# Kernel optimization log

Hardware: AMD Instinct MI355X
Metric: run time of the kernel (lower is better)

## Reference

```python
import jax, jax.numpy as jnp
import numpy as np

N = 50000
E = 800000
DIM = 256
HEADS = 4
HDIM = DIM // HEADS  # 64
NEG_SLOPE = 0.2
LN_EPS = 1e-5


def _layernorm(x, g, b):
    mu = jnp.mean(x, axis=-1, keepdims=True)
    var = jnp.var(x, axis=-1, keepdims=True)
    return (x - mu) * jax.lax.rsqrt(var + LN_EPS) * g + b


def setup_inputs() -> dict:
    key = jax.random.key(0)
    ks = jax.random.split(key, 10)
    x = jax.random.normal(ks[0], (N, DIM), dtype=jnp.float32)
    edge_index = jax.random.randint(ks[1], (2, E), 0, N, dtype=jnp.int64)
    s = 0.05
    W = jax.random.normal(ks[2], (DIM, DIM), dtype=jnp.float32) * s       # GAT linear (heads*out = dim)
    a_src = jax.random.normal(ks[3], (HEADS, HDIM), dtype=jnp.float32) * s
    a_dst = jax.random.normal(ks[4], (HEADS, HDIM), dtype=jnp.float32) * s
    gat_b = jnp.zeros((DIM,), dtype=jnp.float32)
    ln_g = jnp.ones((DIM,), dtype=jnp.float32)
    ln_b = jnp.zeros((DIM,), dtype=jnp.float32)
    W1 = jax.random.normal(ks[5], (DIM, 4 * DIM), dtype=jnp.float32) * s
    b1 = jnp.zeros((4 * DIM,), dtype=jnp.float32)
    W2 = jax.random.normal(ks[6], (4 * DIM, DIM), dtype=jnp.float32) * s
    b2 = jnp.zeros((DIM,), dtype=jnp.float32)
    return {"x": x, "edge_index": edge_index, "W": W, "a_src": a_src,
            "a_dst": a_dst, "gat_b": gat_b, "ln_g": ln_g, "ln_b": ln_b,
            "W1": W1, "b1": b1, "W2": W2, "b2": b2}


def _gat(x, edge_index, W, a_src, a_dst, gat_b):
    # project and split heads: [N, H, C]
    h = (x @ W).reshape(N, HEADS, HDIM)
    alpha_src = jnp.einsum('nhc,hc->nh', h, a_src)  # [N, H]
    alpha_dst = jnp.einsum('nhc,hc->nh', h, a_dst)  # [N, H]
    src = edge_index[0]
    dst = edge_index[1]
    e = jax.nn.leaky_relu(alpha_src[src] + alpha_dst[dst], NEG_SLOPE)  # [E, H]
    # segment softmax over edges sharing a destination node
    m = jax.ops.segment_max(e, dst, num_segments=N)                   # [N, H]
    ex = jnp.exp(e - m[dst])
    denom = jax.ops.segment_sum(ex, dst, num_segments=N)              # [N, H]
    alpha = ex / (denom[dst] + 1e-16)                                 # [E, H]
    msg = h[src] * alpha[:, :, None]                                  # [E, H, C]
    out = jax.ops.segment_sum(msg.reshape(E, DIM), dst, num_segments=N)
    return out + gat_b


def reference(x, edge_index, W, a_src, a_dst, gat_b, ln_g, ln_b, W1, b1, W2, b2):
    residual = x
    g = _gat(x, edge_index, W, a_src, a_dst, gat_b)
    x = _layernorm(x + g, ln_g, ln_b)
    ffn = jax.nn.gelu(x @ W1 + b1, approximate=False) @ W2 + b2
    x = _layernorm(x + ffn, ln_g, ln_b)  # same norm params reused, as in source
    return x + residual
```

## Files before the change

### kernel.cpp

```cpp
#include <hip/hip_runtime.h>
#include <hip/hip_bf16.h>
#include <math.h>

typedef __bf16 bf16;
typedef bf16 bf16x8 __attribute__((ext_vector_type(8)));
typedef float floatx4 __attribute__((ext_vector_type(4)));

#define NN 50000
#define EE 800000
#define DIMC 256
#define FFC 1024

typedef __attribute__((address_space(3))) unsigned int lds_u32;
typedef __attribute__((address_space(1))) unsigned int gbl_u32;

static __device__ __forceinline__ void glds16(const bf16* g, bf16* l) {
    __builtin_amdgcn_global_load_lds((const gbl_u32*)g, (lds_u32*)l, 16, 0, 0);
}

static __device__ __forceinline__ unsigned short f2b(float f) {
    bf16 b = (bf16)f;
    return __builtin_bit_cast(unsigned short, b);
}
static __device__ __forceinline__ float b2f_lo(unsigned u) { return __uint_as_float(u << 16); }
static __device__ __forceinline__ float b2f_hi(unsigned u) { return __uint_as_float(u & 0xffff0000u); }

static __device__ __forceinline__ float gelu_f(float v) {
    float z = -1.5957691216f * v - 0.0713548163f * v * v * v;
    return v / (1.f + __expf(z));
}

__global__ __launch_bounds__(256)
void k_cast_bf16(const float* __restrict__ in, bf16* __restrict__ out, long n4) {
    long i = (long)blockIdx.x * 256 + threadIdx.x;
    if (i >= n4) return;
    float4 v = ((const float4*)in)[i];
    uint2 p;
    p.x = (unsigned)f2b(v.x) | ((unsigned)f2b(v.y) << 16);
    p.y = (unsigned)f2b(v.z) | ((unsigned)f2b(v.w) << 16);
    ((uint2*)out)[i] = p;
}

__global__ __launch_bounds__(256)
void k_tcast(const float* __restrict__ in, bf16* __restrict__ out, int K, int Nc) {
    __shared__ float t[32][33];
    int n0 = blockIdx.x * 32, k0 = blockIdx.y * 32;
    int tx = threadIdx.x & 31, ty = threadIdx.x >> 5;
#pragma unroll
    for (int i = 0; i < 4; ++i)
        t[ty + i * 8][tx] = in[(long)(k0 + ty + i * 8) * Nc + n0 + tx];
    __syncthreads();
#pragma unroll
    for (int i = 0; i < 4; ++i)
        out[(long)(n0 + ty + i * 8) * K + k0 + tx] = (bf16)t[tx][ty + i * 8];
}

template <int EPI>
__global__ __launch_bounds__(256)
void k_gemmA(const bf16* __restrict__ A, const bf16* __restrict__ BT,
             bf16* __restrict__ C, const float* __restrict__ bias,
             const float* __restrict__ avs, const float* __restrict__ avd,
             float* __restrict__ asrcO, float* __restrict__ adstO,
             int M, int K, int Nc) {
    __shared__ __attribute__((aligned(16))) bf16 smem[17408];
    bf16* As = smem;
    bf16* Bs = smem + 8192;
    const int tid = threadIdx.x;
    const int w = tid >> 6, lane = tid & 63;
    const int gm = blockIdx.x * 128, gn = blockIdx.y * 128;
    const int wm = (w >> 1) * 64, wn = (w & 1) * 64;
    const int lr = lane & 15, lkc = lane >> 4;

    long aoff[4], boff[4];
#pragma unroll
    for (int j = 0; j < 4; ++j) {
        int s = w * 4 + j;
        int r = s * 8 + (lane >> 3);
        int kc = ((lane & 7) ^ (r & 7)) * 8;
        aoff[j] = (long)min(gm + r, M - 1) * K + kc;
        boff[j] = (long)(gn + r) * K + kc;
    }

    floatx4 acc[4][4];
#pragma unroll
    for (int a = 0; a < 4; ++a)
#pragma unroll
        for (int b = 0; b < 4; ++b) acc[a][b] = floatx4{0.f, 0.f, 0.f, 0.f};

    for (int k0 = 0; k0 < K; k0 += 64) {
        if (k0) __syncthreads();
#pragma unroll
        for (int j = 0; j < 4; ++j) {
            int s = w * 4 + j;
            glds16(A + aoff[j] + k0, As + s * 512);
            glds16(BT + boff[j] + k0, Bs + s * 512);
        }
        __syncthreads();
#pragma unroll
        for (int kk = 0; kk < 2; ++kk) {
            bf16x8 af[4], bv[4];
#pragma unroll
            for (int mi = 0; mi < 4; ++mi) {
                int r = wm + mi * 16 + lr;
                int ch = (kk * 4 + lkc) ^ (r & 7);
                af[mi] = *(const bf16x8*)(As + r * 64 + ch * 8);
            }
#pragma unroll
            for (int ni = 0; ni < 4; ++ni) {
                int r = wn + ni * 16 + lr;
                int ch = (kk * 4 + lkc) ^ (r & 7);
                bv[ni] = *(const bf16x8*)(Bs + r * 64 + ch * 8);
            }
#pragma unroll
            for (int mi = 0; mi < 4; ++mi)
#pragma unroll
                for (int ni = 0; ni < 4; ++ni)
                    acc[mi][ni] = __builtin_amdgcn_mfma_f32_16x16x32_bf16(af[mi], bv[ni], acc[mi][ni], 0, 0, 0);
        }
    }

    __syncthreads();
    bf16* cs = smem;
#pragma unroll
    for (int ni = 0; ni < 4; ++ni) {
        const int cl = wn + ni * 16 + lr;
        const float bvs = (EPI == 1) ? bias[gn + cl] : 0.f;
#pragma unroll
        for (int mi = 0; mi < 4; ++mi)
#pragma unroll
            for (int i = 0; i < 4; ++i) {
                int rl = wm + mi * 16 + lkc * 4 + i;
                float v = acc[mi][ni][i] + bvs;
                if (EPI == 1) v = gelu_f(v);
                cs[rl * 136 + cl] = (bf16)v;
            }
    }
    __syncthreads();

    const int c8 = (lane & 15) * 8;
    float as8[8], ad8[8];
    int hd = 0;
    if (EPI == 0) {
        hd = (gn >> 6) + ((lane & 15) >> 3);
        const int cb = hd * 64 + (c8 & 63);
#pragma unroll
        for (int i = 0; i < 8; ++i) { as8[i] = avs[cb + i]; ad8[i] = avd[cb + i]; }
    }

#pragma unroll
    for (int t = 0; t < 8; ++t) {
        int rl = w * 32 + t * 4 + (lane >> 4);
        int grow = gm + rl;
        uint4 val = *(const uint4*)(cs + rl * 136 + c8);
        if (grow < M) *(uint4*)(C + (long)grow * Nc + gn + c8) = val;
        if (EPI == 0) {
            float h0 = b2f_lo(val.x), h1 = b2f_hi(val.x), h2 = b2f_lo(val.y), h3 = b2f_hi(val.y);
            float h4 = b2f_lo(val.z), h5 = b2f_hi(val.z), h6 = b2f_lo(val.w), h7 = b2f_hi(val.w);
            float ds = h0 * as8[0] + h1 * as8[1] + h2 * as8[2] + h3 * as8[3]
                     + h4 * as8[4] + h5 * as8[5] + h6 * as8[6] + h7 * as8[7];
            float dd = h0 * ad8[0] + h1 * ad8[1] + h2 * ad8[2] + h3 * ad8[3]
                     + h4 * ad8[4] + h5 * ad8[5] + h6 * ad8[6] + h7 * ad8[7];
#pragma unroll
            for (int off = 1; off < 8; off <<= 1) { ds += __shfl_xor(ds, off); dd += __shfl_xor(dd, off); }
            if ((lane & 7) == 0 && grow < M) {
                asrcO[grow * 4 + hd] = ds;
                adstO[grow * 4 + hd] = dd;
            }
        }
    }
}

__global__ __launch_bounds__(512)
void k_ffn(const bf16* __restrict__ x1b, const bf16* __restrict__ W1T,
           const bf16* __restrict__ W2T, const float* __restrict__ b1,
           const float* __restrict__ b2, const float* __restrict__ x,
           const float* __restrict__ lng, const float* __restrict__ lnb,
           float* __restrict__ out, int M) {
    __shared__ __attribute__((aligned(16))) bf16 smem[20480];
    float* actf = (float*)smem;
    bf16* w1s = smem + 4096;
    bf16* w2s = smem + 12288;
    const int tid = threadIdx.x;
    const int w = tid >> 6, lane = tid & 63;
    const int lr = lane & 15, lkc = lane >> 4;
    const int mg = w >> 1, nh = w & 1;
    const int gm = blockIdx.x * 64;

    bf16x8 xf[8];
    {
        long rb = (long)min(gm + mg * 16 + lr, M - 1) * DIMC;
#pragma unroll
        for (int kf = 0; kf < 8; ++kf)
            xf[kf] = *(const bf16x8*)(x1b + rb + kf * 32 + lkc * 8);
    }

    floatx4 accB[8];
#pragma unroll
    for (int i = 0; i < 8; ++i) accB[i] = floatx4{0.f, 0.f, 0.f, 0.f};

    const int rbA = nh * 16 + lr;
    const int rAct = mg * 16 + lr;
    const int kAct = nh * 16 + lr;

    for (int c = 0; c < 32; ++c) {
        if (c) __syncthreads();
#pragma unroll
        for (int j = 0; j < 2; ++j) {
            int sg = w * 2 + j;
            int r = sg * 2 + (lane >> 5);
            int col = ((lane & 31) ^ (r & 7)) * 8;
            glds16(W1T + (long)(c * 32 + r) * DIMC + col, w1s + sg * 512);
        }
#pragma unroll
        for (int j = 0; j < 2; ++j) {
            int sg = w * 2 + j;
            int r = sg * 16 + (lane >> 2);
            int col = c * 32 + (((lane & 3) ^ ((r >> 1) & 3)) * 8);
            glds16(W2T + (long)r * FFC + col, w2s + sg * 512);
        }
        __syncthreads();

        floatx4 a0 = floatx4{0.f, 0.f, 0.f, 0.f}, a1 = a0;
#pragma unroll
        for (int kf = 0; kf < 8; kf += 2) {
            int g0 = (kf * 4 + lkc) ^ (rbA & 7);
            int g1 = ((kf + 1) * 4 + lkc) ^ (rbA & 7);
            bf16x8 bva = *(const bf16x8*)(w1s + rbA * 256 + g0 * 8);
            bf16x8 bvb = *(const bf16x8*)(w1s + rbA * 256 + g1 * 8);
            a0 = __builtin_amdgcn_mfma_f32_16x16x32_bf16(xf[kf], bva, a0, 0, 0, 0);
            a1 = __builtin_amdgcn_mfma_f32_16x16x32_bf16(xf[kf + 1], bvb, a1, 0, 0, 0);
        }
        float b1v = b1[c * 32 + kAct];
#pragma unroll
        for (int i = 0; i < 4; ++i) {
            int r = mg * 16 + lkc * 4 + i;
            float v = gelu_f(a0[i] + a1[i] + b1v);
            actf[r * 32 + (((kAct >> 2) ^ (r & 7)) << 2) + (kAct & 3)] = v;
        }
        __syncthreads();

        {
            int g0 = (lkc * 2) ^ (rAct & 7);
            int g1 = (lkc * 2 + 1) ^ (rAct & 7);
            float4 lo = *(const float4*)(actf + rAct * 32 + g0 * 4);
            float4 hi = *(const float4*)(actf + rAct * 32 + g1 * 4);
            bf16x8 af;
            af[0] = (bf16)lo.x; af[1] = (bf16)lo.y; af[2] = (bf16)lo.z; af[3] = (bf16)lo.w;
            af[4] = (bf16)hi.x; af[5] = (bf16)hi.y; af[6] = (bf16)hi.z; af[7] = (bf16)hi.w;
#pragma unroll
            for (int ni = 0; ni < 8; ++ni) {
                int rb = nh * 128 + ni * 16 + lr;
                int gb = lkc ^ ((rb >> 1) & 3);
                bf16x8 bv = *(const bf16x8*)(w2s + rb * 32 + gb * 8);
                accB[ni] = __builtin_amdgcn_mfma_f32_16x16x32_bf16(af, bv, accB[ni], 0, 0, 0);
            }
        }
    }

    __syncthreads();
    bf16* cs = smem;
#pragma unroll
    for (int ni = 0; ni < 8; ++ni) {
        int col = nh * 128 + ni * 16 + lr;
        float b2v = b2[col];
#pragma unroll
        for (int i = 0; i < 4; ++i) {
            int rl = mg * 16 + lkc * 4 + i;
            cs[rl * 264 + col] = (bf16)(accB[ni][i] + b2v);
        }
    }
    __syncthreads();
    float4 g4 = *(const float4*)(lng + lane * 4);
    float4 lb4 = *(const float4*)(lnb + lane * 4);
#pragma unroll 1
    for (int t = 0; t < 8; ++t) {
        int r = w * 8 + t;
        int grow = gm + r;
        long base = (long)min(grow, M - 1) * DIMC + lane * 4;
        uint2 cu = *(const uint2*)(cs + r * 264 + lane * 4);
        uint2 xu = *(const uint2*)(x1b + base);
        float v0 = b2f_lo(cu.x) + b2f_lo(xu.x);
        float v1 = b2f_hi(cu.x) + b2f_hi(xu.x);
        float v2 = b2f_lo(cu.y) + b2f_lo(xu.y);
        float v3 = b2f_hi(cu.y) + b2f_hi(xu.y);
        float s1 = v0 + v1 + v2 + v3;
        float s2 = v0 * v0 + v1 * v1 + v2 * v2 + v3 * v3;
#pragma unroll
        for (int off = 1; off < 64; off <<= 1) { s1 += __shfl_xor(s1, off); s2 += __shfl_xor(s2, off); }
        float mu = s1 * (1.f / DIMC);
        float rs = rsqrtf(s2 * (1.f / DIMC) - mu * mu + 1e-5f);
        float4 xr = *(const float4*)(x + base);
        float4 o;
        o.x = (v0 - mu) * rs * g4.x + lb4.x + xr.x;
        o.y = (v1 - mu) * rs * g4.y + lb4.y + xr.y;
        o.z = (v2 - mu) * rs * g4.z + lb4.z + xr.z;
        o.w = (v3 - mu) * rs * g4.w + lb4.w + xr.w;
        if (grow < M) *(float4*)(out + (long)grow * DIMC + lane * 4) = o;
    }
}

__global__ __launch_bounds__(256)
void k_count(const int* __restrict__ dst, unsigned* __restrict__ deg) {
    int e = blockIdx.x * 256 + threadIdx.x;
    if (e < EE) atomicAdd(&deg[dst[e]], 1u);
}

__global__ __launch_bounds__(1024)
void k_scan(const unsigned* __restrict__ deg, unsigned* __restrict__ rowoff,
            unsigned* __restrict__ cursor) {
    __shared__ unsigned wsum[16], wscan[16];
    __shared__ unsigned carry;
    int tid = threadIdx.x, lane = tid & 63, wid = tid >> 6;
    if (tid == 0) carry = 0;
    __syncthreads();
    for (int base = 0; base < NN; base += 1024) {
        int i = base + tid;
        unsigned v = (i < NN) ? deg[i] : 0u;
        unsigned s = v;
        for (int off = 1; off < 64; off <<= 1) {
            unsigned t = __shfl_up(s, off);
            if (lane >= off) s += t;
        }
        if (lane == 63) wsum[wid] = s;
        __syncthreads();
        if (wid == 0) {
            unsigned t = (lane < 16) ? wsum[lane] : 0u;
            unsigned ts = t;
            for (int off = 1; off < 16; off <<= 1) {
                unsigned u2 = __shfl_up(ts, off);
                if (lane >= off) ts += u2;
            }
            if (lane < 16) wscan[lane] = ts;
        }
        __syncthreads();
        unsigned basew = (wid > 0) ? wscan[wid - 1] : 0u;
        unsigned excl = carry + basew + (s - v);
        if (i < NN) { rowoff[i] = excl; cursor[i] = excl; }
        __syncthreads();
        if (tid == 0) carry += wscan[15];
        __syncthreads();
    }
    if (tid == 0) rowoff[NN] = carry;
}

__global__ __launch_bounds__(256)
void k_fill(const int* __restrict__ src, const int* __restrict__ dst,
            unsigned* __restrict__ cursor, unsigned* __restrict__ elist) {
    int e = blockIdx.x * 256 + threadIdx.x;
    if (e < EE) {
        unsigned p = atomicAdd(&cursor[dst[e]], 1u);
        elist[p] = (unsigned)src[e];
    }
}

__global__ __launch_bounds__(256)
void k_agg_ln1(const unsigned* __restrict__ rowoff, const unsigned* __restrict__ elist,
               const float* __restrict__ asrc, const float* __restrict__ adst,
               const bf16* __restrict__ hb, const float* __restrict__ x,
               const float* __restrict__ gatb, const float* __restrict__ lng,
               const float* __restrict__ lnb, bf16* __restrict__ x1b) {
    int node = (blockIdx.x * 256 + threadIdx.x) >> 6;
    int lane = threadIdx.x & 63;
    if (node >= NN) return;
    int beg = (int)rowoff[node], end = (int)rowoff[node + 1];
    int head = lane >> 4;
    float ad = adst[node * 4 + head];
    const int c = lane * 4;
    const bf16* hc = hb + c;
    const int bl = lane & 48;

    float dsum = 0.f;
    float a0 = 0.f, a1 = 0.f, a2 = 0.f, a3 = 0.f;

    for (int c0 = beg; c0 < end; c0 += 16) {
        int take = end - c0; if (take > 16) take = 16;
        int jj = c0 + (lane & 15);
        float ex = 0.f; int s = 0;
        if (jj < end) {
            s = (int)elist[jj];
            float e = asrc[s * 4 + head] + ad;
            e = (e > 0.f) ? e : 0.2f * e;
            ex = __expf(e);
        }
        dsum += ex;
        if (take == 16) {
#pragma unroll
            for (int j = 0; j < 16; ++j) {
                float al = __shfl(ex, bl + j);
                int sj = __shfl(s, bl + j);
                uint2 u = *(const uint2*)(hc + (long)sj * DIMC);
                a0 += al * b2f_lo(u.x);
                a1 += al * b2f_hi(u.x);
                a2 += al * b2f_lo(u.y);
                a3 += al * b2f_hi(u.y);
            }
        } else {
            for (int j = 0; j < take; ++j) {
                float al = __shfl(ex, bl + j);
                int sj = __shfl(s, bl + j);
                uint2 u = *(const uint2*)(hc + (long)sj * DIMC);
                a0 += al * b2f_lo(u.x);
                a1 += al * b2f_hi(u.x);
                a2 += al * b2f_lo(u.y);
                a3 += al * b2f_hi(u.y);
            }
        }
    }
    dsum += __shfl_xor(dsum, 1);
    dsum += __shfl_xor(dsum, 2);
    dsum += __shfl_xor(dsum, 4);
    dsum += __shfl_xor(dsum, 8);
    float invd = 1.f / (dsum + 1e-16f);
    a0 *= invd; a1 *= invd; a2 *= invd; a3 *= invd;

    long base = (long)node * DIMC + c;
    float4 xr = *(const float4*)(x + base);
    float4 gb = *(const float4*)(gatb + c);
    float v0 = xr.x + a0 + gb.x;
    float v1 = xr.y + a1 + gb.y;
    float v2 = xr.z + a2 + gb.z;
    float v3 = xr.w + a3 + gb.w;
    float s1 = v0 + v1 + v2 + v3;
    float s2 = v0 * v0 + v1 * v1 + v2 * v2 + v3 * v3;
    for (int off = 1; off < 64; off <<= 1) { s1 += __shfl_xor(s1, off); s2 += __shfl_xor(s2, off); }
    float mu = s1 * (1.f / DIMC);
    float rs = rsqrtf(s2 * (1.f / DIMC) - mu * mu + 1e-5f);
    float4 g4 = *(const float4*)(lng + c);
    float4 b4 = *(const float4*)(lnb + c);
    float y0 = (v0 - mu) * rs * g4.x + b4.x;
    float y1 = (v1 - mu) * rs * g4.y + b4.y;
    float y2 = (v2 - mu) * rs * g4.z + b4.z;
    float y3 = (v3 - mu) * rs * g4.w + b4.w;
    uint2 p;
    p.x = (unsigned)f2b(y0) | ((unsigned)f2b(y1) << 16);
    p.y = (unsigned)f2b(y2) | ((unsigned)f2b(y3) << 16);
    *(uint2*)(x1b + base) = p;
}

extern "C" void kernel_launch(void* const* d_in, const int* in_sizes, int n_in,
                              void* d_out, int out_size, void* d_ws, size_t ws_size,
                              hipStream_t stream) {
    const float* x    = (const float*)d_in[0];
    const int*   ei   = (const int*)d_in[1];
    const float* W    = (const float*)d_in[2];
    const float* a_s  = (const float*)d_in[3];
    const float* a_d  = (const float*)d_in[4];
    const float* gatb = (const float*)d_in[5];
    const float* lng  = (const float*)d_in[6];
    const float* lnb  = (const float*)d_in[7];
    const float* W1   = (const float*)d_in[8];
    const float* b1   = (const float*)d_in[9];
    const float* W2   = (const float*)d_in[10];
    const float* b2   = (const float*)d_in[11];
    float* out = (float*)d_out;
    char* ws = (char*)d_ws;

    bf16*     xb     = (bf16*)(ws + 0L);
    bf16*     hb     = (bf16*)(ws + 25600000L);
    bf16*     x1b    = (bf16*)(ws + 51200000L);
    float*    asrc   = (float*)(ws + 179200000L);
    float*    adst   = (float*)(ws + 180000000L);
    unsigned* deg    = (unsigned*)(ws + 180800000L);
    unsigned* cursor = (unsigned*)(ws + 181000192L);
    unsigned* rowoff = (unsigned*)(ws + 181200384L);
    unsigned* elist  = (unsigned*)(ws + 181400832L);
    bf16*     WT     = (bf16*)(ws + 184600832L);
    bf16*     W1T    = (bf16*)(ws + 184731904L);
    bf16*     W2T    = (bf16*)(ws + 185256192L);

    const int* esrc = ei;
    const int* edst = ei + EE;

    hipMemsetAsync(deg, 0, NN * sizeof(unsigned), stream);
    k_cast_bf16<<<12500, 256, 0, stream>>>(x, xb, (long)NN * DIMC / 4);
    {
        dim3 gw(DIMC / 32, DIMC / 32);
        k_tcast<<<gw, 256, 0, stream>>>(W, WT, DIMC, DIMC);
        dim3 gw1(FFC / 32, DIMC / 32);
        k_tcast<<<gw1, 256, 0, stream>>>(W1, W1T, DIMC, FFC);
        dim3 gw2(DIMC / 32, FFC / 32);
        k_tcast<<<gw2, 256, 0, stream>>>(W2, W2T, FFC, DIMC);
    }

    dim3 g1(391, 2);
    k_gemmA<0><<<g1, 256, 0, stream>>>(xb, WT, hb, nullptr, a_s, a_d, asrc, adst, NN, DIMC, DIMC);

    k_count<<<3125, 256, 0, stream>>>(edst, deg);
    k_scan<<<1, 1024, 0, stream>>>(deg, rowoff, cursor);
    k_fill<<<3125, 256, 0, stream>>>(esrc, edst, cursor, elist);

    k_agg_ln1<<<12500, 256, 0, stream>>>(rowoff, elist, asrc, adst, hb, x, gatb, lng, lnb, x1b);

    k_ffn<<<782, 512, 0, stream>>>(x1b, W1T, W2T, b1, b2, x, lng, lnb, out, NN);
}
```

Before: 500.9 us.

## Fuse degree count into cast, merge weight transposes, parallelize CSR scan

Folds the per-edge degree atomics into the bf16 cast kernel and merges the three weight-transpose launches into one grid with block-index dispatch. The single-block serial scan over 50000 nodes becomes a three-phase multi-block scan: per-block scan, block-sum scan, then an offset add. This removes several launches and the long single-workgroup scan, at the cost of two extra small kernels and extra rowoff/cursor read-modify-write traffic.

Result: faster. 442.2 us (-11.7%).

```diff
diff --git a/kernel.cpp b/kernel.cpp
--- a/kernel.cpp
+++ b/kernel.cpp
@@ -31,8 +31,10 @@
 }
 
 __global__ __launch_bounds__(256)
-void k_cast_bf16(const float* __restrict__ in, bf16* __restrict__ out, long n4) {
+void k_cast_count(const float* __restrict__ in, bf16* __restrict__ out, long n4,
+                  const int* __restrict__ dst, unsigned* __restrict__ deg) {
     long i = (long)blockIdx.x * 256 + threadIdx.x;
+    if (i < EE) atomicAdd(&deg[dst[(int)i]], 1u);
     if (i >= n4) return;
     float4 v = ((const float4*)in)[i];
     uint2 p;
@@ -42,9 +44,16 @@
 }
 
 __global__ __launch_bounds__(256)
-void k_tcast(const float* __restrict__ in, bf16* __restrict__ out, int K, int Nc) {
+void k_tcast_all(const float* __restrict__ W, bf16* __restrict__ WT,
+                 const float* __restrict__ W1, bf16* __restrict__ W1T,
+                 const float* __restrict__ W2, bf16* __restrict__ W2T) {
     __shared__ float t[32][33];
-    int n0 = blockIdx.x * 32, k0 = blockIdx.y * 32;
+    int b = blockIdx.x;
+    const float* in; bf16* out; int K, Nc, bx, by;
+    if (b < 64)        { in = W;  out = WT;  K = 256;  Nc = 256;  bx = b & 7;  by = b >> 3; }
+    else if (b < 320)  { b -= 64;  in = W1; out = W1T; K = 256;  Nc = 1024; bx = b & 31; by = b >> 5; }
+    else               { b -= 320; in = W2; out = W2T; K = 1024; Nc = 256;  bx = b & 7;  by = b >> 3; }
+    int n0 = bx * 32, k0 = by * 32;
     int tx = threadIdx.x & 31, ty = threadIdx.x >> 5;
 #pragma unroll
     for (int i = 0; i < 4; ++i)
@@ -299,48 +308,58 @@
     }
 }
 
+__global__ __launch_bounds__(1024)
+void k_scan1(const unsigned* __restrict__ deg, unsigned* __restrict__ rowoff,
+             unsigned* __restrict__ cursor, unsigned* __restrict__ bsum) {
+    __shared__ unsigned wsum[16], wscan[16];
+    int tid = threadIdx.x, lane = tid & 63, wid = tid >> 6;
+    int i = blockIdx.x * 1024 + tid;
+    unsigned v = (i < NN) ? deg[i] : 0u;
+    unsigned s = v;
+    for (int off = 1; off < 64; off <<= 1) {
+        unsigned t = __shfl_up(s, off);
+        if (lane >= off) s += t;
+    }
+    if (lane == 63) wsum[wid] = s;
+    __syncthreads();
+    if (wid == 0) {
+        unsigned t = (lane < 16) ? wsum[lane] : 0u;
+        unsigned ts = t;
+        for (int off = 1; off < 16; off <<= 1) {
+            unsigned u2 = __shfl_up(ts, off);
+            if (lane >= off) ts += u2;
+        }
+        if (lane < 16) wscan[lane] = ts;
+    }
+    __syncthreads();
+    unsigned basew = (wid > 0) ? wscan[wid - 1] : 0u;
+    unsigned excl = basew + (s - v);
+    if (i < NN) { rowoff[i] = excl; cursor[i] = excl; }
+    if (tid == 0) bsum[blockIdx.x] = wscan[15];
+}
+
+__global__ __launch_bounds__(64)
+void k_scan2(unsigned* __restrict__ bsum, unsigned* __restrict__ rowoff) {
+    int lane = threadIdx.x;
+    unsigned v = (lane < 49) ? bsum[lane] : 0u;
+    unsigned s = v;
+    for (int off = 1; off < 64; off <<= 1) {
+        unsigned t = __shfl_up(s, off);
+        if (lane >= off) s += t;
+    }
+    if (lane < 49) bsum[lane] = s - v;
+    if (lane == 48) rowoff[NN] = s;
+}
+
 __global__ __launch_bounds__(256)
-void k_count(const int* __restrict__ dst, unsigned* __restrict__ deg) {
-    int e = blockIdx.x * 256 + threadIdx.x;
-    if (e < EE) atomicAdd(&deg[dst[e]], 1u);
-}
-
-__global__ __launch_bounds__(1024)
-void k_scan(const unsigned* __restrict__ deg, unsigned* __restrict__ rowoff,
-            unsigned* __restrict__ cursor) {
-    __shared__ unsigned wsum[16], wscan[16];
-    __shared__ unsigned carry;
-    int tid = threadIdx.x, lane = tid & 63, wid = tid >> 6;
-    if (tid == 0) carry = 0;
-    __syncthreads();
-    for (int base = 0; base < NN; base += 1024) {
-        int i = base + tid;
-        unsigned v = (i < NN) ? deg[i] : 0u;
-        unsigned s = v;
-        for (int off = 1; off < 64; off <<= 1) {
-            unsigned t = __shfl_up(s, off);
-            if (lane >= off) s += t;
-        }
-        if (lane == 63) wsum[wid] = s;
-        __syncthreads();
-        if (wid == 0) {
-            unsigned t = (lane < 16) ? wsum[lane] : 0u;
-            unsigned ts = t;
-            for (int off = 1; off < 16; off <<= 1) {
-                unsigned u2 = __shfl_up(ts, off);
-                if (lane >= off) ts += u2;
-            }
-            if (lane < 16) wscan[lane] = ts;
-        }
-        __syncthreads();
-        unsigned basew = (wid > 0) ? wscan[wid - 1] : 0u;
-        unsigned excl = carry + basew + (s - v);
-        if (i < NN) { rowoff[i] = excl; cursor[i] = excl; }
-        __syncthreads();
-        if (tid == 0) carry += wscan[15];
-        __syncthreads();
-    }
-    if (tid == 0) rowoff[NN] = carry;
+void k_scan3(const unsigned* __restrict__ bsum, unsigned* __restrict__ rowoff,
+             unsigned* __restrict__ cursor) {
+    int i = blockIdx.x * 256 + threadIdx.x;
+    if (i < NN) {
+        unsigned o = bsum[i >> 10];
+        rowoff[i] += o;
+        cursor[i] += o;
+    }
 }
 
 __global__ __launch_bounds__(256)
@@ -458,6 +477,7 @@
     bf16*     xb     = (bf16*)(ws + 0L);
     bf16*     hb     = (bf16*)(ws + 25600000L);
     bf16*     x1b    = (bf16*)(ws + 51200000L);
+    unsigned* bsum   = (unsigned*)(ws + 76800000L);
     float*    asrc   = (float*)(ws + 179200000L);
     float*    adst   = (float*)(ws + 180000000L);
     unsigned* deg    = (unsigned*)(ws + 180800000L);
@@ -472,21 +492,15 @@
     const int* edst = ei + EE;
 
     hipMemsetAsync(deg, 0, NN * sizeof(unsigned), stream);
-    k_cast_bf16<<<12500, 256, 0, stream>>>(x, xb, (long)NN * DIMC / 4);
-    {
-        dim3 gw(DIMC / 32, DIMC / 32);
-        k_tcast<<<gw, 256, 0, stream>>>(W, WT, DIMC, DIMC);
-        dim3 gw1(FFC / 32, DIMC / 32);
-        k_tcast<<<gw1, 256, 0, stream>>>(W1, W1T, DIMC, FFC);
-        dim3 gw2(DIMC / 32, FFC / 32);
-        k_tcast<<<gw2, 256, 0, stream>>>(W2, W2T, FFC, DIMC);
-    }
+    k_cast_count<<<12500, 256, 0, stream>>>(x, xb, (long)NN * DIMC / 4, edst, deg);
+    k_tcast_all<<<576, 256, 0, stream>>>(W, WT, W1, W1T, W2, W2T);
 
     dim3 g1(391, 2);
     k_gemmA<0><<<g1, 256, 0, stream>>>(xb, WT, hb, nullptr, a_s, a_d, asrc, adst, NN, DIMC, DIMC);
 
-    k_count<<<3125, 256, 0, stream>>>(edst, deg);
-    k_scan<<<1, 1024, 0, stream>>>(deg, rowoff, cursor);
+    k_scan1<<<49, 1024, 0, stream>>>(deg, rowoff, cursor, bsum);
+    k_scan2<<<1, 64, 0, stream>>>(bsum, rowoff);
+    k_scan3<<<196, 256, 0, stream>>>(bsum, rowoff, cursor);
     k_fill<<<3125, 256, 0, stream>>>(esrc, edst, cursor, elist);
 
     k_agg_ln1<<<12500, 256, 0, stream>>>(rowoff, elist, asrc, adst, hb, x, gatb, lng, lnb, x1b);
```
